# Optimization experiments

Hardware: AMD Instinct MI355X
Metric: run time of the kernel (lower is better)

The kernel has to match this reference:

```python
import jax, jax.numpy as jnp
import numpy as np

EMBED = 512
HEADS = 8
HEAD_DIM = EMBED // HEADS
SCALE_BASE = 512
NEG = -1e9


def xpos_apply(x, offset, downscale):
    # x: [(b h), L, d]
    L, d = x.shape[1], x.shape[2]
    min_pos = -(L + offset) // 2
    max_pos = L + offset + min_pos
    base = (jnp.arange(0, d, 2, dtype=jnp.float32) + 0.4 * d) / (1.4 * d)      # [d/2]
    power = jnp.arange(min_pos, max_pos, dtype=jnp.float32) / SCALE_BASE        # [L']
    scale = base[None, :] ** power[:, None]                                     # [L', d/2]
    half = d // 2
    inv_freq = 1.0 / (10000.0 ** (jnp.arange(half, dtype=jnp.float32) / half))
    sinusoid = jnp.arange(scale.shape[0], dtype=jnp.float32)[:, None] * inv_freq[None, :]
    sin, cos = jnp.sin(sinusoid), jnp.cos(sinusoid)
    # keep last L rows (no-op when offset == 0)
    scale, sin, cos = scale[-L:], sin[-L:], cos[-L:]
    if downscale:
        scale = 1.0 / scale
    sin2 = jnp.repeat(sin * scale, 2, axis=-1)   # duplicate_interleave -> [L, d]
    cos2 = jnp.repeat(cos * scale, 2, axis=-1)
    x1, x2 = x[..., ::2], x[..., 1::2]
    rot = jnp.stack([-x2, x1], axis=-1).reshape(x.shape)  # rotate_every_two
    return x * cos2[None] + rot * sin2[None]


def split_heads(x, b, L):
    # 'b l (h d) -> (b h) l d'
    return x.reshape(b, L, HEADS, HEAD_DIM).transpose(0, 2, 1, 3).reshape(b * HEADS, L, HEAD_DIM)


def setup_inputs() -> dict:
    key = jax.random.key(0)
    ks = jax.random.split(key, 12)
    b, L = 4, 2048
    inp = {
        'query': jax.random.normal(ks[0], (b, L, EMBED), jnp.float32),
        'key': jax.random.normal(ks[1], (b, L, EMBED), jnp.float32),
        'value': jax.random.normal(ks[2], (b, L, EMBED), jnp.float32),
        'key_padding_mask': jnp.zeros((b, L), jnp.bool_),
        'attn_mask': jnp.where(jnp.tril(jnp.ones((L, L), jnp.bool_)), 0.0, NEG).astype(jnp.float32),
    }
    s = 1.0 / np.sqrt(EMBED)
    inp['Wq'] = jax.random.normal(ks[3], (EMBED, EMBED), jnp.float32) * s
    inp['bq'] = jnp.zeros((EMBED,), jnp.float32)
    inp['Wk'] = jax.random.normal(ks[4], (EMBED, EMBED), jnp.float32) * s
    inp['bk'] = jnp.zeros((EMBED,), jnp.float32)
    inp['Wv'] = jax.random.normal(ks[5], (EMBED, EMBED), jnp.float32) * s
    inp['bv'] = jnp.zeros((EMBED,), jnp.float32)
    inp['Wo'] = jax.random.normal(ks[6], (EMBED, EMBED), jnp.float32) * s
    inp['bo'] = jnp.zeros((EMBED,), jnp.float32)
    return inp


def reference(query, key, value, key_padding_mask, attn_mask, Wq, bq, Wk, bk, Wv, bv, Wo, bo):
    b, L, _ = query.shape
    q = split_heads(query @ Wq.T + bq, b, L)
    k = split_heads(key @ Wk.T + bk, b, L)
    v = split_heads(value @ Wv.T + bv, b, L)
    k = xpos_apply(k, 0, True)
    q = xpos_apply(q, 0, False)
    q = q * (HEAD_DIM ** -0.5)
    aw = jnp.einsum('btd,bsd->bts', q, k)                 # [(b h), t, s]
    aw = jnp.nan_to_num(aw) + attn_mask[None]
    aw = aw.reshape(b, HEADS, L, L)
    aw = jnp.where(key_padding_mask[:, None, None, :], jnp.finfo(aw.dtype).min, aw)
    aw = aw.reshape(b * HEADS, L, L)
    probs = jax.nn.softmax(aw.astype(jnp.float32), axis=-1).astype(aw.dtype)
    attn = jnp.einsum('bts,bsd->btd', probs, v)           # [(b h), t, d]
    attn = attn.reshape(b, HEADS, L, HEAD_DIM).transpose(0, 2, 1, 3).reshape(b, L, EMBED)
    return attn @ Wo.T + bo
```

## Files before the change

kernel.cpp:

```cpp
#include <hip/hip_runtime.h>
#include <hip/hip_bf16.h>

typedef __bf16 bf16x2 __attribute__((ext_vector_type(2)));
typedef __bf16 bf16x4 __attribute__((ext_vector_type(4)));
typedef __bf16 bf16x8 __attribute__((ext_vector_type(8)));
typedef float  f32x4  __attribute__((ext_vector_type(4)));

#define SEQ    2048
#define EMB    512
#define NHEAD  8
#define HD     64
#define NBATCH 4
#define MROWS  (NBATCH*SEQ)
#define QSCALE 0.18033688011112042f
#define INV2PI 0.15915494309189535f
#define TWOPI  6.28318530717958648f
#define NEGFREQ (-0.41524101186092028f)

__device__ __forceinline__ f32x4 mfma16(bf16x8 a, bf16x8 b, f32x4 c) {
  return __builtin_amdgcn_mfma_f32_16x16x32_bf16(a, b, c, 0, 0, 0);
}

typedef __attribute__((address_space(1))) const void gv_t;
typedef __attribute__((address_space(3))) void lv_t;
__device__ __forceinline__ void async16(const void* g, void* l) {
  __builtin_amdgcn_global_load_lds((gv_t*)g, (lv_t*)l, 16, 0, 0);
}

__global__ __launch_bounds__(256) void conv_kernel(const float* __restrict__ q,
                                                   const float* __restrict__ k,
                                                   const float* __restrict__ v,
                                                   const float* __restrict__ wq,
                                                   const float* __restrict__ wk,
                                                   const float* __restrict__ wv,
                                                   const float* __restrict__ wo,
                                                   __bf16* __restrict__ Qf,
                                                   __bf16* __restrict__ Kf,
                                                   __bf16* __restrict__ Vf,
                                                   __bf16* __restrict__ Wb) {
  const int z = blockIdx.y;
  const float* src;
  __bf16* dst;
  size_t i8;
  if (z < 3) {
    src = (z == 0) ? q : (z == 1) ? k : v;
    dst = (z == 0) ? Qf : (z == 1) ? Kf : Vf;
    i8 = ((size_t)blockIdx.x * 256 + threadIdx.x) * 8;
  } else {
    if (blockIdx.x >= 512) return;
    const int zw = blockIdx.x >> 7;
    src = (zw == 0) ? wq : (zw == 1) ? wk : (zw == 2) ? wv : wo;
    dst = Wb + (size_t)zw * (EMB * EMB);
    i8 = ((size_t)(blockIdx.x & 127) * 256 + threadIdx.x) * 8;
  }
  const float4 fa = ((const float4*)(src + i8))[0];
  const float4 fb = ((const float4*)(src + i8))[1];
  bf16x8 h = { (__bf16)fa.x, (__bf16)fa.y, (__bf16)fa.z, (__bf16)fa.w,
               (__bf16)fb.x, (__bf16)fb.y, (__bf16)fb.z, (__bf16)fb.w };
  *(bf16x8*)(dst + i8) = h;
}

__device__ __forceinline__ void gemm_main(const __bf16* __restrict__ A,
                                          const __bf16* __restrict__ W,
                                          __bf16* As, __bf16* Bs,
                                          f32x4 (&acc)[4][4], int m0, int n0) {
  const int tid = threadIdx.x;
  const int wid = tid >> 6, lane = tid & 63;
  const int quad = lane >> 4, l16 = lane & 15;
  const int l7 = l16 & 7;
  const int srow = lane >> 3;
  const int sxor = ((lane & 7) ^ srow) * 8;
  const int wm = (wid >> 1) * 64, wn = (wid & 1) * 64;

  #pragma unroll
  for (int i = 0; i < 4; ++i)
    #pragma unroll
    for (int j = 0; j < 4; ++j) acc[i][j] = (f32x4)(0.0f);

  for (int k0 = 0; k0 < 512; k0 += 64) {
    __syncthreads();
    #pragma unroll
    for (int ii = 0; ii < 4; ++ii) {
      const int r8 = wid * 32 + ii * 8;
      async16(A + (size_t)(m0 + r8 + srow) * 512 + k0 + sxor, &As[r8 * 64]);
      async16(W + (size_t)(n0 + r8 + srow) * 512 + k0 + sxor, &Bs[r8 * 64]);
    }
    __syncthreads();
    #pragma unroll
    for (int ks = 0; ks < 2; ++ks) {
      bf16x8 af[4], bfr[4];
      #pragma unroll
      for (int i = 0; i < 4; ++i)
        af[i] = *(const bf16x8*)&As[(wm + i * 16 + l16) * 64 +
                                    (((quad + ks * 4) ^ l7) * 8)];
      #pragma unroll
      for (int j = 0; j < 4; ++j)
        bfr[j] = *(const bf16x8*)&Bs[(wn + j * 16 + l16) * 64 +
                                     (((quad + ks * 4) ^ l7) * 8)];
      #pragma unroll
      for (int i = 0; i < 4; ++i)
        #pragma unroll
        for (int j = 0; j < 4; ++j)
          acc[i][j] = mfma16(af[i], bfr[j], acc[i][j]);
    }
  }
}

__device__ __forceinline__ void xcd_tile(int& m0, int& n0) {
  const int s = blockIdx.y * 4 + blockIdx.x;
  const int t = s >> 3;
  n0 = (t & 3) * 128;
  m0 = ((s & 7) + ((t >> 2) << 3)) * 128;
}

__global__ __launch_bounds__(256) void gemm_proj_kernel(
    const __bf16* __restrict__ Qf, const __bf16* __restrict__ Kf, const __bf16* __restrict__ Vf,
    const __bf16* __restrict__ Wb,
    const float* __restrict__ bq, const float* __restrict__ bk, const float* __restrict__ bv,
    __bf16* __restrict__ Qx, __bf16* __restrict__ Kx, __bf16* __restrict__ Vt) {
  __shared__ __align__(16) char smem[34816];
  __bf16* As = (__bf16*)smem;
  __bf16* Bs = (__bf16*)(smem + 16384);
  __bf16* T  = (__bf16*)smem;

  const int z = blockIdx.z;
  const __bf16* A = (z == 0) ? Qf : (z == 1) ? Kf : Vf;
  const __bf16* W = Wb + (size_t)z * (EMB * EMB);
  const float* bias = (z == 0) ? bq : (z == 1) ? bk : bv;
  int m0, n0;
  xcd_tile(m0, n0);

  f32x4 acc[4][4];
  gemm_main(A, W, As, Bs, acc, m0, n0);

  const int tid = threadIdx.x;
  const int wid = tid >> 6, lane = tid & 63;
  const int quad = lane >> 4, l16 = lane & 15;
  const int wm = (wid >> 1) * 64, wn = (wid & 1) * 64;

  __syncthreads();

  if (z == 2) {
    #pragma unroll
    for (int j = 0; j < 4; ++j) {
      const float bval = bias[n0 + wn + j * 16 + l16];
      #pragma unroll
      for (int i = 0; i < 4; ++i) {
        bf16x4 p = { (__bf16)(acc[i][j][0] + bval), (__bf16)(acc[i][j][1] + bval),
                     (__bf16)(acc[i][j][2] + bval), (__bf16)(acc[i][j][3] + bval) };
        *(bf16x4*)&T[(wn + j * 16 + l16) * 136 + wm + i * 16 + quad * 4] = p;
      }
    }
    __syncthreads();
    const int nrow = tid >> 1, mh = (tid & 1) << 6;
    bf16x8 vv[8];
    #pragma unroll
    for (int u = 0; u < 8; ++u) vv[u] = *(const bf16x8*)&T[nrow * 136 + mh + u * 8];
    const int n = n0 + nrow, h = n >> 6, d = n & 63;
    const int bb = m0 >> 11, lb2 = (m0 & 2047) + mh;
    __bf16* dst = Vt + ((size_t)(bb * 8 + h) * 64 + d) * 2048 + lb2;
    #pragma unroll
    for (int u = 0; u < 8; ++u) *(bf16x8*)(dst + u * 8) = vv[u];
  } else {
    #pragma unroll
    for (int j = 0; j < 4; ++j) {
      const float bval = bias[n0 + wn + j * 16 + l16];
      #pragma unroll
      for (int i = 0; i < 4; ++i)
        #pragma unroll
        for (int r = 0; r < 4; ++r)
          T[(wm + i * 16 + quad * 4 + r) * 136 + wn + j * 16 + l16] =
              (__bf16)(acc[i][j][r] + bval);
    }
    __syncthreads();
    const int lrow = tid >> 1, half = tid & 1;
    const int gm = m0 + lrow, l = gm & 2047, bb = gm >> 11;
    const int h = (n0 >> 6) + half;
    bf16x8 vv[8];
    #pragma unroll
    for (int u = 0; u < 8; ++u)
      vv[u] = *(const bf16x8*)&T[lrow * 136 + half * 64 + u * 8];
    bf16x8 ov[8];
    const float lf = (float)l;
    const float pw = (lf - 1024.0f) * (1.0f / 512.0f);
    const float qs = (z == 0) ? QSCALE : 1.0f;
    #pragma unroll
    for (int i = 0; i < 32; ++i) {
      const float x1 = (float)vv[i >> 2][(2 * i) & 7];
      const float x2 = (float)vv[i >> 2][(2 * i + 1) & 7];
      const float lb = __log2f((2.0f * i + 25.6f) * (1.0f / 89.6f));
      const float e  = (z == 0) ? (pw * lb) : (-pw * lb);
      const float sc = __builtin_amdgcn_exp2f(e) * qs;
      const float ang = lf * __builtin_amdgcn_exp2f((float)i * NEGFREQ);
      float rev = ang * INV2PI;
      rev -= floorf(rev);
      const float ar = rev * TWOPI;
      const float sn = __sinf(ar) * sc;
      const float cs = __cosf(ar) * sc;
      ov[i >> 2][(2 * i) & 7]     = (__bf16)(x1 * cs - x2 * sn);
      ov[i >> 2][(2 * i + 1) & 7] = (__bf16)(x2 * cs + x1 * sn);
    }
    __bf16* dst = ((z == 0) ? Qx : Kx) + ((size_t)(bb * 8 + h) * 2048 + l) * 64;
    #pragma unroll
    for (int u = 0; u < 8; ++u) *(bf16x8*)(dst + u * 8) = ov[u];
  }
}

__global__ __launch_bounds__(256) void gemm_out_kernel(
    const __bf16* __restrict__ A, const __bf16* __restrict__ W,
    const float* __restrict__ bias, float* __restrict__ C) {
  __shared__ __align__(16) char smem[34816];
  __bf16* As = (__bf16*)smem;
  __bf16* Bs = (__bf16*)(smem + 16384);
  int m0, n0;
  xcd_tile(m0, n0);
  f32x4 acc[4][4];
  gemm_main(A, W, As, Bs, acc, m0, n0);
  const int tid = threadIdx.x;
  const int wid = tid >> 6, lane = tid & 63;
  const int quad = lane >> 4, l16 = lane & 15;
  const int wm = (wid >> 1) * 64, wn = (wid & 1) * 64;
  #pragma unroll
  for (int j = 0; j < 4; ++j) {
    const int n = n0 + wn + j * 16 + l16;
    const float bval = bias[n];
    #pragma unroll
    for (int i = 0; i < 4; ++i)
      #pragma unroll
      for (int r = 0; r < 4; ++r)
        C[(size_t)(m0 + wm + i * 16 + quad * 4 + r) * 512 + n] = acc[i][j][r] + bval;
  }
}

__global__ __launch_bounds__(256) void flash_kernel(const __bf16* __restrict__ Qx,
                                                    const __bf16* __restrict__ Kx,
                                                    const __bf16* __restrict__ Vt,
                                                    const unsigned char* __restrict__ kpm,
                                                    __bf16* __restrict__ Oa) {
  __shared__ __align__(16) __bf16 Ks[2][64 * HD];
  __shared__ __align__(16) __bf16 Vs[2][64 * HD];
  __shared__ __align__(16) __bf16 Qs[64 * HD];

  const int tid = threadIdx.x;
  const int wid = tid >> 6;
  const int lane = tid & 63;
  const int quad = lane >> 4;
  const int l16 = lane & 15;
  const int l7 = l16 & 7;
  const int srow = lane >> 3;
  const int sxor = ((lane & 7) ^ srow) * 8;
  const int bh = blockIdx.x;
  const int b = bh >> 3;
  const int qb = 31 - (int)blockIdx.y;
  const int q0 = qb * 64;

  const __bf16* Qbase = Qx + (size_t)bh * (SEQ * HD);
  const __bf16* Kbase = Kx + (size_t)bh * (SEQ * HD);
  const __bf16* Vbase = Vt + (size_t)bh * (HD * SEQ);
  __bf16* Pw = Qs + wid * 1024;

  #pragma unroll
  for (int ii = 0; ii < 2; ++ii) {
    const int r0 = wid * 16 + ii * 8;
    async16(Qbase + (size_t)(q0 + r0 + srow) * HD + sxor, &Qs[r0 * HD]);
    async16(Kbase + (size_t)(r0 + srow) * HD + sxor, &Ks[0][r0 * HD]);
    async16(Vbase + (size_t)(r0 + srow) * SEQ + sxor, &Vs[0][r0 * HD]);
  }
  __syncthreads();
  const bf16x8 qf0 = *(const bf16x8*)&Qs[(wid * 16 + l16) * HD + ((quad ^ l7) * 8)];
  const bf16x8 qf1 = *(const bf16x8*)&Qs[(wid * 16 + l16) * HD + (((quad + 4) ^ l7) * 8)];

  f32x4 o0 = (f32x4)(0.0f), o1 = (f32x4)(0.0f), o2 = (f32x4)(0.0f), o3 = (f32x4)(0.0f);
  float m_run = -1e30f, l_run = 0.0f;
  const int myq = q0 + wid * 16 + l16;
  const int niter = qb + 1;

  for (int it = 0; it < niter; ++it) {
    const int kv0 = it << 6;
    const int cur = it & 1;
    const __bf16* Kc = &Ks[cur][0];
    const __bf16* Vc = &Vs[cur][0];

    if (it + 1 < niter) {
      const int kn = kv0 + 64;
      #pragma unroll
      for (int ii = 0; ii < 2; ++ii) {
        const int r0 = wid * 16 + ii * 8;
        async16(Kbase + (size_t)(kn + r0 + srow) * HD + sxor, &Ks[cur ^ 1][r0 * HD]);
        async16(Vbase + (size_t)(r0 + srow) * SEQ + kn + sxor, &Vs[cur ^ 1][r0 * HD]);
      }
    }
    const unsigned char* kp0 = kpm + b * SEQ + kv0;
    unsigned pk[4];
    #pragma unroll
    for (int nb = 0; nb < 4; ++nb)
      pk[nb] = *(const unsigned*)(kp0 + nb * 16 + quad * 4);

    f32x4 s[4];
    #pragma unroll
    for (int nb = 0; nb < 4; ++nb) s[nb] = (f32x4)(0.0f);
    __builtin_amdgcn_s_setprio(1);
    #pragma unroll
    for (int nb = 0; nb < 4; ++nb) {
      const bf16x8 kf = *(const bf16x8*)&Kc[(nb * 16 + l16) * HD + ((quad ^ l7) * 8)];
      s[nb] = mfma16(kf, qf0, s[nb]);
    }
    #pragma unroll
    for (int nb = 0; nb < 4; ++nb) {
      const bf16x8 kf = *(const bf16x8*)&Kc[(nb * 16 + l16) * HD + (((quad + 4) ^ l7) * 8)];
      s[nb] = mfma16(kf, qf1, s[nb]);
    }
    __builtin_amdgcn_s_setprio(0);

    if (kv0 + 63 > q0 + wid * 16) {
      #pragma unroll
      for (int nb = 0; nb < 4; ++nb)
        #pragma unroll
        for (int r = 0; r < 4; ++r)
          if (kv0 + nb * 16 + quad * 4 + r > myq) s[nb][r] = -1e30f;
    }
    #pragma unroll
    for (int nb = 0; nb < 4; ++nb) {
      if (pk[nb]) {
        if (pk[nb] & 0x000000FFu) s[nb][0] = -1e30f;
        if (pk[nb] & 0x0000FF00u) s[nb][1] = -1e30f;
        if (pk[nb] & 0x00FF0000u) s[nb][2] = -1e30f;
        if (pk[nb] & 0xFF000000u) s[nb][3] = -1e30f;
      }
    }

    float mx;
    {
      f32x4 u0, u1;
      #pragma unroll
      for (int r = 0; r < 4; ++r) u0[r] = fmaxf(s[0][r], s[1][r]);
      #pragma unroll
      for (int r = 0; r < 4; ++r) u1[r] = fmaxf(s[2][r], s[3][r]);
      #pragma unroll
      for (int r = 0; r < 4; ++r) u0[r] = fmaxf(u0[r], u1[r]);
      mx = fmaxf(fmaxf(u0[0], u0[1]), fmaxf(u0[2], u0[3]));
    }
    mx = fmaxf(mx, __shfl_xor(mx, 16));
    mx = fmaxf(mx, __shfl_xor(mx, 32));
    if (__any(mx > m_run)) {
      const float m_new = fmaxf(m_run, mx);
      const float alpha = __builtin_amdgcn_exp2f(m_run - m_new);
      o0 *= alpha; o1 *= alpha; o2 *= alpha; o3 *= alpha;
      l_run *= alpha;
      m_run = m_new;
    }
    #pragma unroll
    for (int nb = 0; nb < 4; ++nb)
      #pragma unroll
      for (int r = 0; r < 4; ++r)
        s[nb][r] = __builtin_amdgcn_exp2f(s[nb][r] - m_run);
    {
      f32x4 v01 = s[0] + s[1];
      f32x4 v23 = s[2] + s[3];
      f32x4 vt = v01 + v23;
      float ssum = (vt[0] + vt[1]) + (vt[2] + vt[3]);
      ssum += __shfl_xor(ssum, 16);
      ssum += __shfl_xor(ssum, 32);
      l_run += ssum;
    }

    #pragma unroll
    for (int nb = 0; nb < 4; ++nb) {
      bf16x4 p4 = { (__bf16)s[nb][0], (__bf16)s[nb][1],
                    (__bf16)s[nb][2], (__bf16)s[nb][3] };
      *(bf16x4*)&Pw[l16 * 64 + (((nb * 2 + (quad >> 1)) ^ l7) << 3) + (quad & 1) * 4] = p4;
    }

    __builtin_amdgcn_s_setprio(1);
    #pragma unroll
    for (int ks = 0; ks < 2; ++ks) {
      const bf16x8 pf = *(const bf16x8*)&Pw[l16 * 64 + (((ks * 4 + quad) ^ l7) << 3)];
      const int bx = ((quad + ks * 4) ^ l7) * 8;
      o0 = mfma16(*(const bf16x8*)&Vc[( 0 + l16) * HD + bx], pf, o0);
      o1 = mfma16(*(const bf16x8*)&Vc[(16 + l16) * HD + bx], pf, o1);
      o2 = mfma16(*(const bf16x8*)&Vc[(32 + l16) * HD + bx], pf, o2);
      o3 = mfma16(*(const bf16x8*)&Vc[(48 + l16) * HD + bx], pf, o3);
    }
    __builtin_amdgcn_s_setprio(0);

    if (it + 1 < niter) __syncthreads();
  }

  const float inv_l = 1.0f / l_run;
  {
    bf16x4 t0 = { (__bf16)(o0[0] * inv_l), (__bf16)(o0[1] * inv_l),
                  (__bf16)(o0[2] * inv_l), (__bf16)(o0[3] * inv_l) };
    bf16x4 t1 = { (__bf16)(o1[0] * inv_l), (__bf16)(o1[1] * inv_l),
                  (__bf16)(o1[2] * inv_l), (__bf16)(o1[3] * inv_l) };
    bf16x4 t2 = { (__bf16)(o2[0] * inv_l), (__bf16)(o2[1] * inv_l),
                  (__bf16)(o2[2] * inv_l), (__bf16)(o2[3] * inv_l) };
    bf16x4 t3 = { (__bf16)(o3[0] * inv_l), (__bf16)(o3[1] * inv_l),
                  (__bf16)(o3[2] * inv_l), (__bf16)(o3[3] * inv_l) };
    *(bf16x4*)&Pw[l16 * 64 + (((0 + (quad >> 1)) ^ l7) << 3) + (quad & 1) * 4] = t0;
    *(bf16x4*)&Pw[l16 * 64 + (((2 + (quad >> 1)) ^ l7) << 3) + (quad & 1) * 4] = t1;
    *(bf16x4*)&Pw[l16 * 64 + (((4 + (quad >> 1)) ^ l7) << 3) + (quad & 1) * 4] = t2;
    *(bf16x4*)&Pw[l16 * 64 + (((6 + (quad >> 1)) ^ l7) << 3) + (quad & 1) * 4] = t3;
  }
  const int h = bh & 7;
  #pragma unroll
  for (int ii = 0; ii < 2; ++ii) {
    const int qr = ii * 8 + (lane >> 3);
    const bf16x8 ovv = *(const bf16x8*)&Pw[qr * 64 + (((lane & 7) ^ (qr & 7)) << 3)];
    *(bf16x8*)(Oa + (((size_t)b * SEQ + q0 + wid * 16 + qr) * NHEAD + h) * HD +
               (lane & 7) * 8) = ovv;
  }
}

extern "C" void kernel_launch(void* const* d_in, const int* in_sizes, int n_in,
                              void* d_out, int out_size, void* d_ws, size_t ws_size,
                              hipStream_t stream) {
  (void)in_sizes; (void)n_in; (void)out_size; (void)ws_size;
  const float* query = (const float*)d_in[0];
  const float* key   = (const float*)d_in[1];
  const float* value = (const float*)d_in[2];
  const unsigned char* kpm = (const unsigned char*)d_in[3];
  const float* Wq = (const float*)d_in[5];
  const float* bq = (const float*)d_in[6];
  const float* Wk = (const float*)d_in[7];
  const float* bk = (const float*)d_in[8];
  const float* Wv = (const float*)d_in[9];
  const float* bv = (const float*)d_in[10];
  const float* Wo = (const float*)d_in[11];
  const float* bo = (const float*)d_in[12];
  float* out = (float*)d_out;

  char* ws = (char*)d_ws;
  const size_t SZ = (size_t)MROWS * EMB * 2;
  __bf16* Qf = (__bf16*)(ws);
  __bf16* Kf = (__bf16*)(ws + SZ);
  __bf16* Vf = (__bf16*)(ws + 2 * SZ);
  __bf16* Qx = (__bf16*)(ws + 3 * SZ);
  __bf16* Kx = (__bf16*)(ws + 4 * SZ);
  __bf16* Vt = (__bf16*)(ws + 5 * SZ);
  __bf16* Wb = (__bf16*)(ws + 6 * SZ);
  __bf16* Oa = Qf;

  conv_kernel<<<dim3(2048, 4), dim3(256), 0, stream>>>(
      query, key, value, Wq, Wk, Wv, Wo, Qf, Kf, Vf, Wb);
  gemm_proj_kernel<<<dim3(4, 64, 3), dim3(256), 0, stream>>>(
      Qf, Kf, Vf, Wb, bq, bk, bv, Qx, Kx, Vt);
  flash_kernel<<<dim3(32, 32), dim3(256), 0, stream>>>(Qx, Kx, Vt, kpm, Oa);
  gemm_out_kernel<<<dim3(4, 64), dim3(256), 0, stream>>>(
      Oa, Wb + (size_t)3 * EMB * EMB, bo, out);
}
```

Before: 210.1 us.

## Unroll flash loop by two and defer softmax row reductions

```diff
diff --git a/kernel.cpp b/kernel.cpp
--- a/kernel.cpp
+++ b/kernel.cpp
@@ -267,139 +267,173 @@
     async16(Vbase + (size_t)(r0 + srow) * SEQ + sxor, &Vs[0][r0 * HD]);
   }
   __syncthreads();
-  const bf16x8 qf0 = *(const bf16x8*)&Qs[(wid * 16 + l16) * HD + ((quad ^ l7) * 8)];
-  const bf16x8 qf1 = *(const bf16x8*)&Qs[(wid * 16 + l16) * HD + (((quad + 4) ^ l7) * 8)];
-
-  f32x4 o0 = (f32x4)(0.0f), o1 = (f32x4)(0.0f), o2 = (f32x4)(0.0f), o3 = (f32x4)(0.0f);
+
+  const int base0 = (quad ^ l7) * 8;
+  const int base1 = ((quad + 4) ^ l7) * 8;
+  const int kvo0 = l16 * 64 + base0;
+  const int kvo1 = l16 * 64 + base1;
+
+  const bf16x8 qf0 = *(const bf16x8*)&Qs[(wid * 16 + l16) * HD + base0];
+  const bf16x8 qf1 = *(const bf16x8*)&Qs[(wid * 16 + l16) * HD + base1];
+
+  __bf16* const pw0 = Pw + l16 * 64 + (((0 + (quad >> 1)) ^ l7) << 3) + (quad & 1) * 4;
+  __bf16* const pw1 = Pw + l16 * 64 + (((2 + (quad >> 1)) ^ l7) << 3) + (quad & 1) * 4;
+  __bf16* const pw2 = Pw + l16 * 64 + (((4 + (quad >> 1)) ^ l7) << 3) + (quad & 1) * 4;
+  __bf16* const pw3 = Pw + l16 * 64 + (((6 + (quad >> 1)) ^ l7) << 3) + (quad & 1) * 4;
+  const __bf16* const pr0 = Pw + kvo0;
+  const __bf16* const pr1 = Pw + kvo1;
+
+  f32x4 o[4];
+  #pragma unroll
+  for (int i = 0; i < 4; ++i) o[i] = (f32x4)(0.0f);
+  const f32x4 z4 = (f32x4)(0.0f);
   float m_run = -1e30f, l_run = 0.0f;
   const int myq = q0 + wid * 16 + l16;
   const int niter = qb + 1;
 
-  for (int it = 0; it < niter; ++it) {
-    const int kv0 = it << 6;
-    const int cur = it & 1;
-    const __bf16* Kc = &Ks[cur][0];
-    const __bf16* Vc = &Vs[cur][0];
-
-    if (it + 1 < niter) {
-      const int kn = kv0 + 64;
-      #pragma unroll
-      for (int ii = 0; ii < 2; ++ii) {
-        const int r0 = wid * 16 + ii * 8;
-        async16(Kbase + (size_t)(kn + r0 + srow) * HD + sxor, &Ks[cur ^ 1][r0 * HD]);
-        async16(Vbase + (size_t)(r0 + srow) * SEQ + kn + sxor, &Vs[cur ^ 1][r0 * HD]);
-      }
-    }
-    const unsigned char* kp0 = kpm + b * SEQ + kv0;
-    unsigned pk[4];
-    #pragma unroll
-    for (int nb = 0; nb < 4; ++nb)
-      pk[nb] = *(const unsigned*)(kp0 + nb * 16 + quad * 4);
-
-    f32x4 s[4];
-    #pragma unroll
-    for (int nb = 0; nb < 4; ++nb) s[nb] = (f32x4)(0.0f);
-    __builtin_amdgcn_s_setprio(1);
-    #pragma unroll
-    for (int nb = 0; nb < 4; ++nb) {
-      const bf16x8 kf = *(const bf16x8*)&Kc[(nb * 16 + l16) * HD + ((quad ^ l7) * 8)];
-      s[nb] = mfma16(kf, qf0, s[nb]);
-    }
-    #pragma unroll
-    for (int nb = 0; nb < 4; ++nb) {
-      const bf16x8 kf = *(const bf16x8*)&Kc[(nb * 16 + l16) * HD + (((quad + 4) ^ l7) * 8)];
-      s[nb] = mfma16(kf, qf1, s[nb]);
-    }
-    __builtin_amdgcn_s_setprio(0);
-
-    if (kv0 + 63 > q0 + wid * 16) {
-      #pragma unroll
-      for (int nb = 0; nb < 4; ++nb)
-        #pragma unroll
-        for (int r = 0; r < 4; ++r)
-          if (kv0 + nb * 16 + quad * 4 + r > myq) s[nb][r] = -1e30f;
-    }
-    #pragma unroll
-    for (int nb = 0; nb < 4; ++nb) {
-      if (pk[nb]) {
-        if (pk[nb] & 0x000000FFu) s[nb][0] = -1e30f;
-        if (pk[nb] & 0x0000FF00u) s[nb][1] = -1e30f;
-        if (pk[nb] & 0x00FF0000u) s[nb][2] = -1e30f;
-        if (pk[nb] & 0xFF000000u) s[nb][3] = -1e30f;
-      }
-    }
-
-    float mx;
-    {
-      f32x4 u0, u1;
-      #pragma unroll
-      for (int r = 0; r < 4; ++r) u0[r] = fmaxf(s[0][r], s[1][r]);
-      #pragma unroll
-      for (int r = 0; r < 4; ++r) u1[r] = fmaxf(s[2][r], s[3][r]);
-      #pragma unroll
-      for (int r = 0; r < 4; ++r) u0[r] = fmaxf(u0[r], u1[r]);
-      mx = fmaxf(fmaxf(u0[0], u0[1]), fmaxf(u0[2], u0[3]));
-    }
-    mx = fmaxf(mx, __shfl_xor(mx, 16));
-    mx = fmaxf(mx, __shfl_xor(mx, 32));
-    if (__any(mx > m_run)) {
-      const float m_new = fmaxf(m_run, mx);
-      const float alpha = __builtin_amdgcn_exp2f(m_run - m_new);
-      o0 *= alpha; o1 *= alpha; o2 *= alpha; o3 *= alpha;
-      l_run *= alpha;
-      m_run = m_new;
-    }
-    #pragma unroll
-    for (int nb = 0; nb < 4; ++nb)
-      #pragma unroll
-      for (int r = 0; r < 4; ++r)
-        s[nb][r] = __builtin_amdgcn_exp2f(s[nb][r] - m_run);
-    {
-      f32x4 v01 = s[0] + s[1];
-      f32x4 v23 = s[2] + s[3];
-      f32x4 vt = v01 + v23;
-      float ssum = (vt[0] + vt[1]) + (vt[2] + vt[3]);
-      ssum += __shfl_xor(ssum, 16);
-      ssum += __shfl_xor(ssum, 32);
-      l_run += ssum;
-    }
-
-    #pragma unroll
-    for (int nb = 0; nb < 4; ++nb) {
-      bf16x4 p4 = { (__bf16)s[nb][0], (__bf16)s[nb][1],
-                    (__bf16)s[nb][2], (__bf16)s[nb][3] };
-      *(bf16x4*)&Pw[l16 * 64 + (((nb * 2 + (quad >> 1)) ^ l7) << 3) + (quad & 1) * 4] = p4;
-    }
-
-    __builtin_amdgcn_s_setprio(1);
-    #pragma unroll
-    for (int ks = 0; ks < 2; ++ks) {
-      const bf16x8 pf = *(const bf16x8*)&Pw[l16 * 64 + (((ks * 4 + quad) ^ l7) << 3)];
-      const int bx = ((quad + ks * 4) ^ l7) * 8;
-      o0 = mfma16(*(const bf16x8*)&Vc[( 0 + l16) * HD + bx], pf, o0);
-      o1 = mfma16(*(const bf16x8*)&Vc[(16 + l16) * HD + bx], pf, o1);
-      o2 = mfma16(*(const bf16x8*)&Vc[(32 + l16) * HD + bx], pf, o2);
-      o3 = mfma16(*(const bf16x8*)&Vc[(48 + l16) * HD + bx], pf, o3);
-    }
-    __builtin_amdgcn_s_setprio(0);
-
-    if (it + 1 < niter) __syncthreads();
-  }
-
-  const float inv_l = 1.0f / l_run;
+  const __bf16* kp0 = Kbase + (size_t)(64 + wid * 16 + srow) * HD + sxor;
+  const __bf16* kp1 = kp0 + 8 * HD;
+  const __bf16* vp0 = Vbase + (size_t)(wid * 16 + srow) * SEQ + 64 + sxor;
+  const __bf16* vp1 = vp0 + 8 * SEQ;
+  const unsigned char* kpmb = kpm + b * SEQ + (l16 << 2);
+
+  int it = 0;
+
+#define FLASH_STEP(CUR)                                                        \
+  {                                                                            \
+    const int kv0 = it << 6;                                                   \
+    if (it + 1 < niter) {                                                      \
+      async16(kp0, &Ks[1 - (CUR)][(wid * 16 + 0) * HD]);                       \
+      async16(kp1, &Ks[1 - (CUR)][(wid * 16 + 8) * HD]);                       \
+      async16(vp0, &Vs[1 - (CUR)][(wid * 16 + 0) * HD]);                       \
+      async16(vp1, &Vs[1 - (CUR)][(wid * 16 + 8) * HD]);                       \
+      kp0 += 64 * HD; kp1 += 64 * HD; vp0 += 64; vp1 += 64;                    \
+    }                                                                          \
+    const unsigned mine = *(const unsigned*)kpmb;                              \
+    f32x4 s[4];                                                                \
+    __builtin_amdgcn_s_setprio(1);                                             \
+    s[0] = mfma16(*(const bf16x8*)&Ks[CUR][kvo0 +    0], qf0, z4);             \
+    s[1] = mfma16(*(const bf16x8*)&Ks[CUR][kvo0 + 1024], qf0, z4);             \
+    s[2] = mfma16(*(const bf16x8*)&Ks[CUR][kvo0 + 2048], qf0, z4);             \
+    s[3] = mfma16(*(const bf16x8*)&Ks[CUR][kvo0 + 3072], qf0, z4);             \
+    s[0] = mfma16(*(const bf16x8*)&Ks[CUR][kvo1 +    0], qf1, s[0]);           \
+    s[1] = mfma16(*(const bf16x8*)&Ks[CUR][kvo1 + 1024], qf1, s[1]);           \
+    s[2] = mfma16(*(const bf16x8*)&Ks[CUR][kvo1 + 2048], qf1, s[2]);           \
+    s[3] = mfma16(*(const bf16x8*)&Ks[CUR][kvo1 + 3072], qf1, s[3]);           \
+    __builtin_amdgcn_s_setprio(0);                                             \
+                    \
+    if (kv0 + 63 > q0 + wid * 16) {                                            \
+      _Pragma("unroll")                                                        \
+      for (int nb = 0; nb < 4; ++nb)                                           \
+        _Pragma("unroll")                                                      \
+        for (int r = 0; r < 4; ++r)                                            \
+          if (kv0 + nb * 16 + quad * 4 + r > myq) s[nb][r] = -1e30f;           \
+    }                                                                          \
+                   \
+    if (__any(mine != 0)) {                                                    \
+      const unsigned char* kq = kpm + b * SEQ + kv0;                           \
+      _Pragma("unroll")                                                        \
+      for (int nb = 0; nb < 4; ++nb) {                                         \
+        const unsigned pk = *(const unsigned*)(kq + nb * 16 + quad * 4);       \
+        if (pk) {                                                              \
+          if (pk & 0x000000FFu) s[nb][0] = -1e30f;                             \
+          if (pk & 0x0000FF00u) s[nb][1] = -1e30f;                             \
+          if (pk & 0x00FF0000u) s[nb][2] = -1e30f;                             \
+          if (pk & 0xFF000000u) s[nb][3] = -1e30f;                             \
+        }                                                                      \
+      }                                                                        \
+    }                                                                          \
+                      \
+    float mx;                                                                  \
+    {                                                                          \
+      f32x4 u0, u1;                                                            \
+      _Pragma("unroll")                                                        \
+      for (int r = 0; r < 4; ++r) u0[r] = fmaxf(s[0][r], s[1][r]);             \
+      _Pragma("unroll")                                                        \
+      for (int r = 0; r < 4; ++r) u1[r] = fmaxf(s[2][r], s[3][r]);             \
+      _Pragma("unroll")                                                        \
+      for (int r = 0; r < 4; ++r) u0[r] = fmaxf(u0[r], u1[r]);                 \
+      mx = fmaxf(fmaxf(u0[0], u0[1]), fmaxf(u0[2], u0[3]));                    \
+    }                                                                          \
+    if (__any(mx > m_run)) {                                                   \
+      float rm = fmaxf(mx, __shfl_xor(mx, 16));                                \
+      rm = fmaxf(rm, __shfl_xor(rm, 32));                                      \
+      const float m_new = fmaxf(m_run, rm);                                    \
+      const float alpha = __builtin_amdgcn_exp2f(m_run - m_new);               \
+      o[0] *= alpha; o[1] *= alpha; o[2] *= alpha; o[3] *= alpha;              \
+      l_run *= alpha;                                                          \
+      m_run = m_new;                                                           \
+    }                                                                          \
+    _Pragma("unroll")                                                          \
+    for (int nb = 0; nb < 4; ++nb)                                             \
+      _Pragma("unroll")                                                        \
+      for (int r = 0; r < 4; ++r)                                              \
+        s[nb][r] = __builtin_amdgcn_exp2f(s[nb][r] - m_run);                   \
+    {                                                                          \
+      f32x4 v01 = s[0] + s[1];                                                 \
+      f32x4 v23 = s[2] + s[3];                                                 \
+      f32x4 vt = v01 + v23;                                                    \
+      l_run += (vt[0] + vt[1]) + (vt[2] + vt[3]);                              \
+    }                                                                          \
+           \
+    *(bf16x4*)pw0 = bf16x4{ (__bf16)s[0][0], (__bf16)s[0][1],                  \
+                            (__bf16)s[0][2], (__bf16)s[0][3] };                \
+    *(bf16x4*)pw1 = bf16x4{ (__bf16)s[1][0], (__bf16)s[1][1],                  \
+                            (__bf16)s[1][2], (__bf16)s[1][3] };                \
+    *(bf16x4*)pw2 = bf16x4{ (__bf16)s[2][0], (__bf16)s[2][1],                  \
+                            (__bf16)s[2][2], (__bf16)s[2][3] };                \
+    *(bf16x4*)pw3 = bf16x4{ (__bf16)s[3][0], (__bf16)s[3][1],                  \
+                            (__bf16)s[3][2], (__bf16)s[3][3] };                \
+                                     \
+    {                                                                          \
+      const bf16x8 pf0 = *(const bf16x8*)pr0;                                  \
+      __builtin_amdgcn_s_setprio(1);                                           \
+      o[0] = mfma16(*(const bf16x8*)&Vs[CUR][kvo0 +    0], pf0, o[0]);         \
+      o[1] = mfma16(*(const bf16x8*)&Vs[CUR][kvo0 + 1024], pf0, o[1]);         \
+      o[2] = mfma16(*(const bf16x8*)&Vs[CUR][kvo0 + 2048], pf0, o[2]);         \
+      o[3] = mfma16(*(const bf16x8*)&Vs[CUR][kvo0 + 3072], pf0, o[3]);         \
+      __builtin_amdgcn_s_setprio(0);                                           \
+      const bf16x8 pf1 = *(const bf16x8*)pr1;                                  \
+      __builtin_amdgcn_s_setprio(1);                                           \
+      o[0] = mfma16(*(const bf16x8*)&Vs[CUR][kvo1 +    0], pf1, o[0]);         \
+      o[1] = mfma16(*(const bf16x8*)&Vs[CUR][kvo1 + 1024], pf1, o[1]);         \
+      o[2] = mfma16(*(const bf16x8*)&Vs[CUR][kvo1 + 2048], pf1, o[2]);         \
+      o[3] = mfma16(*(const bf16x8*)&Vs[CUR][kvo1 + 3072], pf1, o[3]);         \
+      __builtin_amdgcn_s_setprio(0);                                           \
+    }                                                                          \
+    kpmb += 64;                                                                \
+      \
+    if (it + 1 < niter) __syncthreads();                                       \
+  }
+
+  while (it + 1 < niter) {
+    FLASH_STEP(0);
+    ++it;
+    FLASH_STEP(1);
+    ++it;
+  }
+  if (it < niter) {
+    FLASH_STEP(0);
+  }
+#undef FLASH_STEP
+
+  float lt = l_run + __shfl_xor(l_run, 16);
+  lt += __shfl_xor(lt, 32);
+
+  const float inv_l = 1.0f / lt;
   {
-    bf16x4 t0 = { (__bf16)(o0[0] * inv_l), (__bf16)(o0[1] * inv_l),
-                  (__bf16)(o0[2] * inv_l), (__bf16)(o0[3] * inv_l) };
-    bf16x4 t1 = { (__bf16)(o1[0] * inv_l), (__bf16)(o1[1] * inv_l),
-                  (__bf16)(o1[2] * inv_l), (__bf16)(o1[3] * inv_l) };
-    bf16x4 t2 = { (__bf16)(o2[0] * inv_l), (__bf16)(o2[1] * inv_l),
-                  (__bf16)(o2[2] * inv_l), (__bf16)(o2[3] * inv_l) };
-    bf16x4 t3 = { (__bf16)(o3[0] * inv_l), (__bf16)(o3[1] * inv_l),
-                  (__bf16)(o3[2] * inv_l), (__bf16)(o3[3] * inv_l) };
-    *(bf16x4*)&Pw[l16 * 64 + (((0 + (quad >> 1)) ^ l7) << 3) + (quad & 1) * 4] = t0;
-    *(bf16x4*)&Pw[l16 * 64 + (((2 + (quad >> 1)) ^ l7) << 3) + (quad & 1) * 4] = t1;
-    *(bf16x4*)&Pw[l16 * 64 + (((4 + (quad >> 1)) ^ l7) << 3) + (quad & 1) * 4] = t2;
-    *(bf16x4*)&Pw[l16 * 64 + (((6 + (quad >> 1)) ^ l7) << 3) + (quad & 1) * 4] = t3;
+    bf16x4 t0 = { (__bf16)(o[0][0] * inv_l), (__bf16)(o[0][1] * inv_l),
+                  (__bf16)(o[0][2] * inv_l), (__bf16)(o[0][3] * inv_l) };
+    bf16x4 t1 = { (__bf16)(o[1][0] * inv_l), (__bf16)(o[1][1] * inv_l),
+                  (__bf16)(o[1][2] * inv_l), (__bf16)(o[1][3] * inv_l) };
+    bf16x4 t2 = { (__bf16)(o[2][0] * inv_l), (__bf16)(o[2][1] * inv_l),
+                  (__bf16)(o[2][2] * inv_l), (__bf16)(o[2][3] * inv_l) };
+    bf16x4 t3 = { (__bf16)(o[3][0] * inv_l), (__bf16)(o[3][1] * inv_l),
+                  (__bf16)(o[3][2] * inv_l), (__bf16)(o[3][3] * inv_l) };
+    *(bf16x4*)pw0 = t0;
+    *(bf16x4*)pw1 = t1;
+    *(bf16x4*)pw2 = t2;
+    *(bf16x4*)pw3 = t3;
   }
   const int h = bh & 7;
   #pragma unroll
```

Measured after the change: 206.8 us. No clear change (-1.5%).
